# Performance work log

Measured on AMD Instinct MI355X. Metric: run time of the kernel, lower is better.

## Reference

```python
import jax, jax.numpy as jnp
import numpy as np

B, L, D1, D2 = 4, 2048, 1024, 1024

def setup_inputs() -> dict:
    key = jax.random.key(0)
    k1, k2, k3, k4, k5, k6 = jax.random.split(key, 6)
    s1 = 1.0 / np.sqrt(D1)
    s2 = 1.0 / np.sqrt(D2)
    return {
        "features_1": jax.random.normal(k1, (B, L, D1), dtype=jnp.float32),
        "features_2": jax.random.normal(k2, (B, L, D2), dtype=jnp.float32),
        # nn.Linear(d1, d2): W1 [d2, d1], b1 [d2]
        "W1": jax.random.uniform(k3, (D2, D1), jnp.float32, -s1, s1),
        "b1": jax.random.uniform(k4, (D2,), jnp.float32, -s1, s1),
        # nn.Linear(d2, d1): W2 [d1, d2], b2 [d1]
        "W2": jax.random.uniform(k5, (D1, D2), jnp.float32, -s2, s2),
        "b2": jax.random.uniform(k6, (D1,), jnp.float32, -s2, s2),
    }

def reference(features_1, features_2, W1, b1, W2, b2):
    # transformed_features_1: [B, L, D2]
    t1 = jnp.einsum('bld,ed->ble', features_1, W1) + b1
    # unscaled similarity: [B, L, L]
    sim = jnp.einsum('ble,bme->blm', t1, features_2)
    attn = jax.nn.softmax(sim, axis=-1)  # both softmaxes are identical
    attended_1 = jnp.einsum('blm,bme->ble', attn, features_2)  # [B, L, D2]
    attended_2 = jnp.einsum('blm,bme->ble', attn, t1)          # [B, L, D2]
    attended_2 = jnp.einsum('ble,de->bld', attended_2, W2) + b2  # [B, L, D1]
    return attended_1, attended_2
```

## Files before the change

### kernel.cpp

```cpp
#include <hip/hip_runtime.h>
#include <stdint.h>

#define BB 4
#define LL 2048
#define DD 1024

typedef __attribute__((ext_vector_type(4))) float f32x4;
typedef __attribute__((ext_vector_type(8))) _Float16 f16x8;
typedef __attribute__((ext_vector_type(4))) unsigned short u16x4;
typedef __attribute__((ext_vector_type(8))) unsigned short u16x8;
typedef unsigned short u16;

__device__ __forceinline__ u16 f2h(float x){
  return __builtin_bit_cast(u16, (_Float16)x);
}

__device__ __forceinline__ void gload16(const u16* g, u16* l){
  __builtin_amdgcn_global_load_lds((const __attribute__((address_space(1))) unsigned*)g,
                                   (__attribute__((address_space(3))) unsigned*)l,
                                   16, 0, 0);
}

__device__ __forceinline__ int xcd_swz(int bx, int nwg){
  return (bx & 7) * (nwg >> 3) + (bx >> 3);
}

__device__ __forceinline__ void stage_tile8(u16* lds, const u16* src, int ld, int wave, int lane){
  const int r0 = lane >> 3;
  const int cs = (((lane & 7) ^ r0) << 3);
  #pragma unroll
  for (int j = 0; j < 2; ++j){
    const int rb = wave*16 + j*8;
    gload16(src + (size_t)(rb + r0)*ld + cs, lds + rb*64);
  }
}

__device__ __forceinline__ void stage_fatA(u16* lds, const u16* src, int ld, int wave, int lane){
  const int r0 = lane >> 3;
  const int cs = (((lane & 7) ^ r0) << 3);
  #pragma unroll
  for (int j = 0; j < 8; ++j){
    const int rb = wave*64 + j*8;
    gload16(src + (size_t)(rb + r0)*ld + cs, lds + rb*64);
  }
}
__device__ __forceinline__ void stage_fatB(u16* lds, const u16* src, int ld, int wave, int lane){
  const int r0 = lane >> 3;
  const int cs = (((lane & 7) ^ r0) << 3);
  #pragma unroll
  for (int j = 0; j < 4; ++j){
    const int rb = wave*32 + j*8;
    gload16(src + (size_t)(rb + r0)*ld + cs, lds + rb*64);
  }
}

__device__ __forceinline__ f16x8 frag_ld(const u16* t, int row, int ko){
  return __builtin_bit_cast(f16x8,
    *reinterpret_cast<const f32x4*>(t + row*64 + (ko ^ ((row & 7) << 3))));
}

__global__ void cast3_k(const float* __restrict__ f1, u16* __restrict__ f1f,
                        const float* __restrict__ W1, u16* __restrict__ w1f,
                        const float* __restrict__ W2, u16* __restrict__ w2f){
  const int n1 = (BB*LL*DD)/4, nw = (DD*DD)/4;
  const int stride = gridDim.x * blockDim.x;
  for (int i = blockIdx.x*blockDim.x + threadIdx.x; i < n1 + 2*nw; i += stride){
    const float* s; u16* d; int k;
    if (i < n1){ s = f1; d = f1f; k = i; }
    else if (i < n1 + nw){ s = W1; d = w1f; k = i - n1; }
    else { s = W2; d = w2f; k = i - n1 - nw; }
    f32x4 v = reinterpret_cast<const f32x4*>(s)[k];
    u16x4 h;
    #pragma unroll
    for (int j = 0; j < 4; ++j) h[j] = f2h(v[j]);
    reinterpret_cast<u16x4*>(d)[k] = h;
  }
}

__global__ void castT_k(const float* __restrict__ f2, u16* __restrict__ f2f,
                        u16* __restrict__ f2T){
  __shared__ u16 t[32][33];
  const int b = blockIdx.z;
  const int d0 = blockIdx.x*32, l0 = blockIdx.y*32;
  const float* src = f2 + (size_t)b*LL*DD;
  u16* d1 = f2f + (size_t)b*LL*DD;
  u16* d2 = f2T + (size_t)b*DD*LL;
  const int x = threadIdx.x;
  for (int j = threadIdx.y; j < 32; j += 8){
    u16 h = f2h(src[(size_t)(l0+j)*DD + d0 + x]);
    d1[(size_t)(l0+j)*DD + d0 + x] = h;
    t[j][x] = h;
  }
  __syncthreads();
  for (int j = threadIdx.y; j < 32; j += 8)
    d2[(size_t)(d0+j)*LL + l0 + x] = t[x][j];
}

__global__ __launch_bounds__(512,4) void gemm_t1_k(
    const u16* __restrict__ A_g, const u16* __restrict__ B_g,
    const float* __restrict__ bias, u16* __restrict__ Oh){
  __shared__ __align__(16) u16 As[128*64];
  __shared__ __align__(16) u16 Bs[128*64];
  const int bx = xcd_swz(blockIdx.x, gridDim.x);
  const int bm = bx >> 3, bn = bx & 7;
  const int tid = threadIdx.x, wave = tid>>6, lane = tid&63;
  const int wr = wave>>2, wc = wave&3;
  const u16* Ab = A_g + (size_t)(bm*128)*DD;
  const u16* Bb = B_g + (size_t)(bn*128)*DD;
  f32x4 acc[4][2];
  #pragma unroll
  for (int i=0;i<4;i++)
    #pragma unroll
    for (int j=0;j<2;j++) acc[i][j] = (f32x4){0.f,0.f,0.f,0.f};

  for (int k0 = 0; k0 < DD; k0 += 64){
    __syncthreads();
    stage_tile8(As, Ab + k0, DD, wave, lane);
    stage_tile8(Bs, Bb + k0, DD, wave, lane);
    __syncthreads();
    #pragma unroll
    for (int kk=0;kk<2;kk++){
      const int ko = kk*32 + ((lane>>4)<<3);
      f16x8 a[4], bb[2];
      #pragma unroll
      for (int mi=0;mi<4;mi++) a[mi]  = frag_ld(As, wr*64 + mi*16 + (lane&15), ko);
      #pragma unroll
      for (int ni=0;ni<2;ni++) bb[ni] = frag_ld(Bs, wc*32 + ni*16 + (lane&15), ko);
      #pragma unroll
      for (int mi=0;mi<4;mi++)
        #pragma unroll
        for (int ni=0;ni<2;ni++)
          acc[mi][ni] = __builtin_amdgcn_mfma_f32_16x16x32_f16(a[mi], bb[ni], acc[mi][ni], 0,0,0);
    }
  }
  #pragma unroll
  for (int mi=0;mi<4;mi++)
    #pragma unroll
    for (int ni=0;ni<2;ni++){
      const int r = bm*128 + wr*64 + mi*16 + ((lane>>4)<<2);
      const int c = bn*128 + wc*32 + ni*16 + (lane&15);
      const float bv = bias[c];
      #pragma unroll
      for (int j=0;j<4;j++)
        Oh[(size_t)(r+j)*DD + c] = f2h(acc[mi][ni][j] + bv);
    }
}

__global__ __launch_bounds__(512,4) void gemm_zt_k(const u16* __restrict__ t1f,
                                                   const u16* __restrict__ w2f,
                                                   u16* __restrict__ ZT){
  __shared__ __align__(16) u16 As[128*64];
  __shared__ __align__(16) u16 Bs[128*64];
  __shared__ u16 T[128*132];
  const int bx = xcd_swz(blockIdx.x, gridDim.x);
  const int bm = bx >> 3, bn = bx & 7;
  const int tid = threadIdx.x, wave = tid>>6, lane = tid&63;
  const int wr = wave>>2, wc = wave&3;
  const u16* Ab = t1f + (size_t)(bm*128)*DD;
  const u16* Bb = w2f + (size_t)(bn*128)*DD;
  f32x4 acc[4][2];
  #pragma unroll
  for (int i=0;i<4;i++)
    #pragma unroll
    for (int j=0;j<2;j++) acc[i][j] = (f32x4){0.f,0.f,0.f,0.f};

  for (int k0 = 0; k0 < DD; k0 += 64){
    __syncthreads();
    stage_tile8(As, Ab + k0, DD, wave, lane);
    stage_tile8(Bs, Bb + k0, DD, wave, lane);
    __syncthreads();
    #pragma unroll
    for (int kk=0;kk<2;kk++){
      const int ko = kk*32 + ((lane>>4)<<3);
      f16x8 a[4], bb[2];
      #pragma unroll
      for (int mi=0;mi<4;mi++) a[mi]  = frag_ld(As, wr*64 + mi*16 + (lane&15), ko);
      #pragma unroll
      for (int ni=0;ni<2;ni++) bb[ni] = frag_ld(Bs, wc*32 + ni*16 + (lane&15), ko);
      #pragma unroll
      for (int mi=0;mi<4;mi++)
        #pragma unroll
        for (int ni=0;ni<2;ni++)
          acc[mi][ni] = __builtin_amdgcn_mfma_f32_16x16x32_f16(a[mi], bb[ni], acc[mi][ni], 0,0,0);
    }
  }
  #pragma unroll
  for (int mi=0;mi<4;mi++)
    #pragma unroll
    for (int ni=0;ni<2;ni++){
      const int r = wr*64 + mi*16 + ((lane>>4)<<2);
      const int c = wc*32 + ni*16 + (lane&15);
      #pragma unroll
      for (int j=0;j<4;j++)
        T[(r+j)*132 + c] = f2h(acc[mi][ni][j]);
    }
  __syncthreads();
  const int b2i = bm >> 4;
  const int mb  = (bm*128) & 2047;
  const int d   = tid >> 2, m0 = (tid & 3) << 5;
  u16* dst = ZT + ((size_t)b2i*DD + bn*128 + d)*LL + mb + m0;
  #pragma unroll
  for (int g = 0; g < 4; ++g){
    u16x8 v;
    #pragma unroll
    for (int e = 0; e < 8; ++e) v[e] = T[(m0 + g*8 + e)*132 + d];
    *reinterpret_cast<u16x8*>(dst + g*8) = v;
  }
}

__global__ __launch_bounds__(256) void softmax_k(float* __restrict__ sim){
  const int row = blockIdx.x;
  float* p = sim + (size_t)row * LL;
  const int tid = threadIdx.x, wave = tid>>6, lane = tid&63;
  f32x4 x0 = reinterpret_cast<const f32x4*>(p)[tid];
  f32x4 x1 = reinterpret_cast<const f32x4*>(p)[tid + 256];
  float mx = fmaxf(fmaxf(fmaxf(x0[0],x0[1]), fmaxf(x0[2],x0[3])),
                   fmaxf(fmaxf(x1[0],x1[1]), fmaxf(x1[2],x1[3])));
  #pragma unroll
  for (int o = 32; o; o >>= 1) mx = fmaxf(mx, __shfl_xor(mx, o, 64));
  __shared__ float red[8];
  if (lane == 0) red[wave] = mx;
  __syncthreads();
  mx = fmaxf(fmaxf(red[0], red[1]), fmaxf(red[2], red[3]));
  float e0[4], e1[4], s = 0.f;
  #pragma unroll
  for (int j=0;j<4;j++){ e0[j] = __expf(x0[j]-mx); s += e0[j]; }
  #pragma unroll
  for (int j=0;j<4;j++){ e1[j] = __expf(x1[j]-mx); s += e1[j]; }
  #pragma unroll
  for (int o = 32; o; o >>= 1) s += __shfl_xor(s, o, 64);
  if (lane == 0) red[4+wave] = s;
  __syncthreads();
  s = (red[4]+red[5]) + (red[6]+red[7]);
  const float inv = 1.0f / s;
  u16* ob = reinterpret_cast<u16*>(p);
  u16x4 w0, w1;
  #pragma unroll
  for (int j=0;j<4;j++){ w0[j] = f2h(e0[j]*inv); w1[j] = f2h(e1[j]*inv); }
  reinterpret_cast<u16x4*>(ob)[tid]       = w0;
  reinterpret_cast<u16x4*>(ob)[tid + 256] = w1;
}

template<int EPI>
__global__ __launch_bounds__(256,2) void gemmf_k(
    const u16* __restrict__ A_g, long long sAb, int lda,
    const u16* __restrict__ B0_g, const u16* __restrict__ B1_g, long long sBb, int ldb,
    float* __restrict__ C0, float* __restrict__ C1, long long sCb, int ldc,
    const float* __restrict__ bias, int K, int tn_sh){
  __shared__ __align__(16) u16 As[256*64];
  __shared__ __align__(16) u16 Bs[128*64];
  const int b = blockIdx.y;
  const int bx = xcd_swz(blockIdx.x, gridDim.x);
  const int bm = bx >> tn_sh, bn = bx & ((1 << tn_sh) - 1);
  const int tid = threadIdx.x, wave = tid>>6, lane = tid&63;
  const int wm = wave >> 1, wn = wave & 1;
  const u16* Ab = A_g + (size_t)b*sAb + (size_t)(bm*256)*lda;
  const u16* Bb;
  if (EPI == 0){
    Bb = B0_g + (size_t)b*sBb + (size_t)(bn*128)*ldb;
  } else {
    Bb = ((bn < 8) ? B0_g : B1_g) + (size_t)b*sBb + (size_t)((bn&7)*128)*ldb;
  }
  f32x4 acc[8][4];
  #pragma unroll
  for (int i=0;i<8;i++)
    #pragma unroll
    for (int j=0;j<4;j++) acc[i][j] = (f32x4){0.f,0.f,0.f,0.f};

  for (int k0 = 0; k0 < K; k0 += 64){
    __syncthreads();
    stage_fatA(As, Ab + k0, lda, wave, lane);
    stage_fatB(Bs, Bb + k0, ldb, wave, lane);
    __syncthreads();
    #pragma unroll
    for (int kk=0;kk<2;kk++){
      const int ko = kk*32 + ((lane>>4)<<3);
      f16x8 af[8], bf[4];
      #pragma unroll
      for (int mi=0;mi<8;mi++) af[mi] = frag_ld(As, wm*128 + mi*16 + (lane&15), ko);
      #pragma unroll
      for (int ni=0;ni<4;ni++) bf[ni] = frag_ld(Bs, wn*64 + ni*16 + (lane&15), ko);
      #pragma unroll
      for (int mi=0;mi<8;mi++)
        #pragma unroll
        for (int ni=0;ni<4;ni++)
          acc[mi][ni] = __builtin_amdgcn_mfma_f32_16x16x32_f16(af[mi], bf[ni], acc[mi][ni], 0,0,0);
    }
  }

  if (EPI == 0){
    float* Cb = C0 + (size_t)b*sCb;
    #pragma unroll
    for (int mi=0;mi<8;mi++)
      #pragma unroll
      for (int ni=0;ni<4;ni++){
        const int r = bm*256 + wm*128 + mi*16 + ((lane>>4)<<2);
        const int c = bn*128 + wn*64 + ni*16 + (lane&15);
        #pragma unroll
        for (int j=0;j<4;j++)
          Cb[(size_t)(r+j)*ldc + c] = acc[mi][ni][j];
      }
  } else {
    float* O = ((bn < 8) ? C0 : C1) + (size_t)b*sCb;
    const bool has_bias = (bn >= 8);
    #pragma unroll
    for (int mi=0;mi<8;mi++)
      #pragma unroll
      for (int ni=0;ni<4;ni++){
        const int r = bm*256 + wm*128 + mi*16 + ((lane>>4)<<2);
        const int c = (bn&7)*128 + wn*64 + ni*16 + (lane&15);
        const float bv = has_bias ? bias[c] : 0.f;
        #pragma unroll
        for (int j=0;j<4;j++)
          O[(size_t)(r+j)*ldc + c] = acc[mi][ni][j] + bv;
      }
  }
}

extern "C" void kernel_launch(void* const* d_in, const int* in_sizes, int n_in,
                              void* d_out, int out_size, void* d_ws, size_t ws_size,
                              hipStream_t stream) {
  const float* f1 = (const float*)d_in[0];
  const float* f2 = (const float*)d_in[1];
  const float* W1 = (const float*)d_in[2];
  const float* b1 = (const float*)d_in[3];
  const float* W2 = (const float*)d_in[4];
  const float* b2 = (const float*)d_in[5];
  float* out1 = (float*)d_out;
  float* out2 = out1 + (size_t)BB*LL*DD;

  char* ws = (char*)d_ws;
  u16* t1f = (u16*)(ws + 0);
  u16* ZT  = (u16*)(ws + 16777216);
  u16* f2f = (u16*)(ws + 33554432);
  u16* f2T = (u16*)(ws + 50331648);
  u16* w1f = (u16*)(ws + 67108864);
  u16* w2f = (u16*)(ws + 69206016);
  float* sim = (float*)(ws + 71303168);
  u16* f1f = (u16*)(ws + 71303168);

  castT_k<<<dim3(32, 64, BB), dim3(32, 8), 0, stream>>>(f2, f2f, f2T);
  cast3_k<<<4096, 256, 0, stream>>>(f1, f1f, W1, w1f, W2, w2f);
  gemm_t1_k<<<dim3(512, 1), 512, 0, stream>>>(f1f, w1f, b1, t1f);
  gemmf_k<0><<<dim3(128, BB), 256, 0, stream>>>(t1f, (long long)LL*DD, DD,
                                                f2f, nullptr, (long long)LL*DD, DD,
                                                sim, nullptr, (long long)LL*LL, LL,
                                                nullptr, DD, 4);
  softmax_k<<<BB*LL, 256, 0, stream>>>(sim);
  gemm_zt_k<<<dim3(512, 1), 512, 0, stream>>>(t1f, w2f, ZT);
  gemmf_k<1><<<dim3(128, BB), 256, 0, stream>>>((const u16*)sim, (long long)LL*4096, 4096,
                                                f2T, ZT, (long long)DD*LL, LL,
                                                out1, out2, (long long)LL*DD, DD,
                                                b2, LL, 4);
}
```

Measured before the change: 194.8 us.

## Prefetch next K-tile in gemmf_k by preloading A fragments and double-buffering B

Restructures the gemmf_k main loop so each wave first loads all A fragments for the current K tile into registers. It then issues the async global-to-LDS loads for the next A tile and the next B tile while running MFMAs on the current B buffer. B is double-buffered in shared memory, while A reuses a single buffer because its fragments are already held in registers. The aim is to overlap global memory latency with compute, at the cost of more VGPRs (16 A fragments held) and more LDS, which may lower occupancy under launch_bounds(256,2).

```diff
diff --git a/kernel.cpp b/kernel.cpp
--- a/kernel.cpp
+++ b/kernel.cpp
@@ -248,7 +248,7 @@
     float* __restrict__ C0, float* __restrict__ C1, long long sCb, int ldc,
     const float* __restrict__ bias, int K, int tn_sh){
   __shared__ __align__(16) u16 As[256*64];
-  __shared__ __align__(16) u16 Bs[128*64];
+  __shared__ __align__(16) u16 Bs[2][128*64];
   const int b = blockIdx.y;
   const int bx = xcd_swz(blockIdx.x, gridDim.x);
   const int bm = bx >> tn_sh, bn = bx & ((1 << tn_sh) - 1);
@@ -267,25 +267,37 @@
     #pragma unroll
     for (int j=0;j<4;j++) acc[i][j] = (f32x4){0.f,0.f,0.f,0.f};
 
-  for (int k0 = 0; k0 < K; k0 += 64){
-    __syncthreads();
-    stage_fatA(As, Ab + k0, lda, wave, lane);
-    stage_fatB(Bs, Bb + k0, ldb, wave, lane);
-    __syncthreads();
-    #pragma unroll
-    for (int kk=0;kk<2;kk++){
-      const int ko = kk*32 + ((lane>>4)<<3);
-      f16x8 af[8], bf[4];
-      #pragma unroll
-      for (int mi=0;mi<8;mi++) af[mi] = frag_ld(As, wm*128 + mi*16 + (lane&15), ko);
-      #pragma unroll
-      for (int ni=0;ni<4;ni++) bf[ni] = frag_ld(Bs, wn*64 + ni*16 + (lane&15), ko);
+  const int NT = K >> 6;
+  stage_fatA(As, Ab, lda, wave, lane);
+  stage_fatB(Bs[0], Bb, ldb, wave, lane);
+  __syncthreads();
+
+  for (int t = 0; t < NT; ++t){
+    f16x8 af[8][2];
+    #pragma unroll
+    for (int mi=0;mi<8;mi++)
+      #pragma unroll
+      for (int ks=0;ks<2;ks++)
+        af[mi][ks] = frag_ld(As, wm*128 + mi*16 + (lane&15), ks*32 + ((lane>>4)<<3));
+    __syncthreads();
+    if (t+1 < NT){
+      stage_fatA(As, Ab + (t+1)*64, lda, wave, lane);
+      stage_fatB(Bs[(t+1)&1], Bb + (t+1)*64, ldb, wave, lane);
+    }
+    const u16* Bcur = Bs[t&1];
+    #pragma unroll
+    for (int ks=0;ks<2;ks++){
+      const int ko = ks*32 + ((lane>>4)<<3);
+      f16x8 bf[4];
+      #pragma unroll
+      for (int ni=0;ni<4;ni++) bf[ni] = frag_ld(Bcur, wn*64 + ni*16 + (lane&15), ko);
       #pragma unroll
       for (int mi=0;mi<8;mi++)
         #pragma unroll
         for (int ni=0;ni<4;ni++)
-          acc[mi][ni] = __builtin_amdgcn_mfma_f32_16x16x32_f16(af[mi], bf[ni], acc[mi][ni], 0,0,0);
-    }
+          acc[mi][ni] = __builtin_amdgcn_mfma_f32_16x16x32_f16(af[mi][ks], bf[ni], acc[mi][ni], 0,0,0);
+    }
+    __syncthreads();
   }
 
   if (EPI == 0){
```

Result: slower. 198.7 us (+2.0%).

## Replace batched GEMMs with 8-wave 256x256 double-buffered pipelined kernel

Applied to the files above, without the earlier changes.

Replaces the 256x128-tile, 4-wave, single-buffered batched GEMM used for the similarity and attention-output products with a 256x256-tile, 8-wave kernel. The new kernel double-buffers the LDS tiles and splits each K step into four phases that interleave async global-to-LDS loads with MFMA bursts, using barriers, waitcnt and setprio. The aim is to hide global load latency and raise arithmetic intensity per block. The cost is 128KB of LDS per block and fewer blocks in the grid, which lowers occupancy and tail granularity.

```diff
diff --git a/kernel.cpp b/kernel.cpp
--- a/kernel.cpp
+++ b/kernel.cpp
@@ -31,25 +31,6 @@
   #pragma unroll
   for (int j = 0; j < 2; ++j){
     const int rb = wave*16 + j*8;
-    gload16(src + (size_t)(rb + r0)*ld + cs, lds + rb*64);
-  }
-}
-
-__device__ __forceinline__ void stage_fatA(u16* lds, const u16* src, int ld, int wave, int lane){
-  const int r0 = lane >> 3;
-  const int cs = (((lane & 7) ^ r0) << 3);
-  #pragma unroll
-  for (int j = 0; j < 8; ++j){
-    const int rb = wave*64 + j*8;
-    gload16(src + (size_t)(rb + r0)*ld + cs, lds + rb*64);
-  }
-}
-__device__ __forceinline__ void stage_fatB(u16* lds, const u16* src, int ld, int wave, int lane){
-  const int r0 = lane >> 3;
-  const int cs = (((lane & 7) ^ r0) << 3);
-  #pragma unroll
-  for (int j = 0; j < 4; ++j){
-    const int rb = wave*32 + j*8;
     gload16(src + (size_t)(rb + r0)*ld + cs, lds + rb*64);
   }
 }
@@ -242,50 +223,109 @@
 }
 
 template<int EPI>
-__global__ __launch_bounds__(256,2) void gemmf_k(
+__global__ __launch_bounds__(512,2) void gemm8_k(
     const u16* __restrict__ A_g, long long sAb, int lda,
     const u16* __restrict__ B0_g, const u16* __restrict__ B1_g, long long sBb, int ldb,
     float* __restrict__ C0, float* __restrict__ C1, long long sCb, int ldc,
-    const float* __restrict__ bias, int K, int tn_sh){
-  __shared__ __align__(16) u16 As[256*64];
-  __shared__ __align__(16) u16 Bs[128*64];
+    const float* __restrict__ bias, int K){
+  __shared__ __align__(16) u16 As[2][256*64];
+  __shared__ __align__(16) u16 Bs[2][256*64];
   const int b = blockIdx.y;
   const int bx = xcd_swz(blockIdx.x, gridDim.x);
-  const int bm = bx >> tn_sh, bn = bx & ((1 << tn_sh) - 1);
+  const int bm = bx >> 3, bn = bx & 7;
   const int tid = threadIdx.x, wave = tid>>6, lane = tid&63;
-  const int wm = wave >> 1, wn = wave & 1;
+  const int wm = wave >> 2, wn = wave & 3;
   const u16* Ab = A_g + (size_t)b*sAb + (size_t)(bm*256)*lda;
-  const u16* Bb;
-  if (EPI == 0){
-    Bb = B0_g + (size_t)b*sBb + (size_t)(bn*128)*ldb;
-  } else {
-    Bb = ((bn < 8) ? B0_g : B1_g) + (size_t)b*sBb + (size_t)((bn&7)*128)*ldb;
-  }
+  const u16* Bb = (EPI == 0)
+      ? (B0_g + (size_t)b*sBb + (size_t)(bn*256)*ldb)
+      : (((bn < 4) ? B0_g : B1_g) + (size_t)b*sBb + (size_t)((bn&3)*256)*ldb);
   f32x4 acc[8][4];
   #pragma unroll
   for (int i=0;i<8;i++)
     #pragma unroll
     for (int j=0;j<4;j++) acc[i][j] = (f32x4){0.f,0.f,0.f,0.f};
 
-  for (int k0 = 0; k0 < K; k0 += 64){
-    __syncthreads();
-    stage_fatA(As, Ab + k0, lda, wave, lane);
-    stage_fatB(Bs, Bb + k0, ldb, wave, lane);
-    __syncthreads();
-    #pragma unroll
-    for (int kk=0;kk<2;kk++){
-      const int ko = kk*32 + ((lane>>4)<<3);
-      f16x8 af[8], bf[4];
-      #pragma unroll
-      for (int mi=0;mi<8;mi++) af[mi] = frag_ld(As, wm*128 + mi*16 + (lane&15), ko);
-      #pragma unroll
-      for (int ni=0;ni<4;ni++) bf[ni] = frag_ld(Bs, wn*64 + ni*16 + (lane&15), ko);
-      #pragma unroll
-      for (int mi=0;mi<8;mi++)
-        #pragma unroll
-        for (int ni=0;ni<4;ni++)
-          acc[mi][ni] = __builtin_amdgcn_mfma_f32_16x16x32_f16(af[mi], bf[ni], acc[mi][ni], 0,0,0);
-    }
+  const int NT = K >> 6;
+  auto stA = [&](int tt, int h){
+    stage_tile8(&As[tt&1][h*8192], Ab + (size_t)(h*128)*lda + tt*64, lda, wave, lane);
+  };
+  auto stB = [&](int tt, int h){
+    stage_tile8(&Bs[tt&1][h*8192], Bb + (size_t)(h*128)*ldb + tt*64, ldb, wave, lane);
+  };
+
+  stA(0,0); stB(0,0); stA(0,1); stB(0,1);
+  stA(1,0); stB(1,0);
+  asm volatile("s_waitcnt vmcnt(4)" ::: "memory");
+  __builtin_amdgcn_s_barrier();
+
+  for (int t = 0; t < NT; ++t){
+    const u16* Ap = As[t&1];
+    const u16* Bp = Bs[t&1];
+    const int ar = wm*128 + (lane&15);
+    const int br = wn*64 + (lane&15);
+    const int k0 = ((lane>>4)<<3);
+    const int k1 = 32 + k0;
+    f16x8 af0[8], af1[8], bf0[4], bf1[4];
+
+    #pragma unroll
+    for (int mi=0;mi<8;mi++) af0[mi] = frag_ld(Ap, ar + mi*16, k0);
+    #pragma unroll
+    for (int ni=0;ni<4;ni++) bf0[ni] = frag_ld(Bp, br + ni*16, k0);
+    if (t+1 < NT) stA(t+1, 1);
+    __builtin_amdgcn_s_barrier();
+    asm volatile("s_waitcnt lgkmcnt(0)" ::: "memory");
+    __builtin_amdgcn_sched_barrier(0);
+    __builtin_amdgcn_s_setprio(1);
+    #pragma unroll
+    for (int mi=0;mi<4;mi++)
+      #pragma unroll
+      for (int ni=0;ni<4;ni++)
+        acc[mi][ni] = __builtin_amdgcn_mfma_f32_16x16x32_f16(af0[mi], bf0[ni], acc[mi][ni], 0,0,0);
+    __builtin_amdgcn_s_setprio(0);
+    __builtin_amdgcn_s_barrier();
+
+    #pragma unroll
+    for (int mi=0;mi<8;mi++) af1[mi] = frag_ld(Ap, ar + mi*16, k1);
+    if (t+1 < NT) stB(t+1, 1);
+    __builtin_amdgcn_s_barrier();
+    asm volatile("s_waitcnt lgkmcnt(0)" ::: "memory");
+    __builtin_amdgcn_sched_barrier(0);
+    __builtin_amdgcn_s_setprio(1);
+    #pragma unroll
+    for (int mi=4;mi<8;mi++)
+      #pragma unroll
+      for (int ni=0;ni<4;ni++)
+        acc[mi][ni] = __builtin_amdgcn_mfma_f32_16x16x32_f16(af0[mi], bf0[ni], acc[mi][ni], 0,0,0);
+    __builtin_amdgcn_s_setprio(0);
+    __builtin_amdgcn_s_barrier();
+
+    #pragma unroll
+    for (int ni=0;ni<4;ni++) bf1[ni] = frag_ld(Bp, br + ni*16, k1);
+    if (t+2 < NT) stA(t+2, 0);
+    __builtin_amdgcn_s_barrier();
+    asm volatile("s_waitcnt lgkmcnt(0)" ::: "memory");
+    __builtin_amdgcn_sched_barrier(0);
+    __builtin_amdgcn_s_setprio(1);
+    #pragma unroll
+    for (int mi=0;mi<4;mi++)
+      #pragma unroll
+      for (int ni=0;ni<4;ni++)
+        acc[mi][ni] = __builtin_amdgcn_mfma_f32_16x16x32_f16(af1[mi], bf1[ni], acc[mi][ni], 0,0,0);
+    __builtin_amdgcn_s_setprio(0);
+    __builtin_amdgcn_s_barrier();
+
+    if (t+2 < NT){ stB(t+2, 0); asm volatile("s_waitcnt vmcnt(4)" ::: "memory"); }
+    else         {              asm volatile("s_waitcnt vmcnt(0)" ::: "memory"); }
+    __builtin_amdgcn_s_barrier();
+    __builtin_amdgcn_sched_barrier(0);
+    __builtin_amdgcn_s_setprio(1);
+    #pragma unroll
+    for (int mi=4;mi<8;mi++)
+      #pragma unroll
+      for (int ni=0;ni<4;ni++)
+        acc[mi][ni] = __builtin_amdgcn_mfma_f32_16x16x32_f16(af1[mi], bf1[ni], acc[mi][ni], 0,0,0);
+    __builtin_amdgcn_s_setprio(0);
+    __builtin_amdgcn_s_barrier();
   }
 
   if (EPI == 0){
@@ -295,20 +335,20 @@
       #pragma unroll
       for (int ni=0;ni<4;ni++){
         const int r = bm*256 + wm*128 + mi*16 + ((lane>>4)<<2);
-        const int c = bn*128 + wn*64 + ni*16 + (lane&15);
+        const int c = bn*256 + wn*64 + ni*16 + (lane&15);
         #pragma unroll
         for (int j=0;j<4;j++)
           Cb[(size_t)(r+j)*ldc + c] = acc[mi][ni][j];
       }
   } else {
-    float* O = ((bn < 8) ? C0 : C1) + (size_t)b*sCb;
-    const bool has_bias = (bn >= 8);
+    float* O = ((bn < 4) ? C0 : C1) + (size_t)b*sCb;
+    const bool has_bias = (bn >= 4);
     #pragma unroll
     for (int mi=0;mi<8;mi++)
       #pragma unroll
       for (int ni=0;ni<4;ni++){
         const int r = bm*256 + wm*128 + mi*16 + ((lane>>4)<<2);
-        const int c = (bn&7)*128 + wn*64 + ni*16 + (lane&15);
+        const int c = (bn&3)*256 + wn*64 + ni*16 + (lane&15);
         const float bv = has_bias ? bias[c] : 0.f;
         #pragma unroll
         for (int j=0;j<4;j++)
@@ -342,14 +382,14 @@
   castT_k<<<dim3(32, 64, BB), dim3(32, 8), 0, stream>>>(f2, f2f, f2T);
   cast3_k<<<4096, 256, 0, stream>>>(f1, f1f, W1, w1f, W2, w2f);
   gemm_t1_k<<<dim3(512, 1), 512, 0, stream>>>(f1f, w1f, b1, t1f);
-  gemmf_k<0><<<dim3(128, BB), 256, 0, stream>>>(t1f, (long long)LL*DD, DD,
-                                                f2f, nullptr, (long long)LL*DD, DD,
-                                                sim, nullptr, (long long)LL*LL, LL,
-                                                nullptr, DD, 4);
+  gemm8_k<0><<<dim3(64, BB), 512, 0, stream>>>(t1f, (long long)LL*DD, DD,
+                                               f2f, nullptr, (long long)LL*DD, DD,
+                                               sim, nullptr, (long long)LL*LL, LL,
+                                               nullptr, DD);
   softmax_k<<<BB*LL, 256, 0, stream>>>(sim);
   gemm_zt_k<<<dim3(512, 1), 512, 0, stream>>>(t1f, w2f, ZT);
-  gemmf_k<1><<<dim3(128, BB), 256, 0, stream>>>((const u16*)sim, (long long)LL*4096, 4096,
-                                                f2T, ZT, (long long)DD*LL, LL,
-                                                out1, out2, (long long)LL*DD, DD,
-                                                b2, LL, 4);
-}
+  gemm8_k<1><<<dim3(64, BB), 512, 0, stream>>>((const u16*)sim, (long long)LL*4096, 4096,
+                                               f2T, ZT, (long long)DD*LL, LL,
+                                               out1, out2, (long long)LL*DD, DD,
+                                               b2, LL);
+}
```

After: 201.8 us. +3.6%, slower.

## Store similarity matrix in fp16 and merge the cast kernels into one launch

Applied to the files above, without the earlier changes.

The similarity GEMM now writes fp16 logits instead of fp32, and softmax reads and writes fp16 in place. This halves the traffic of the largest intermediate and makes the PV GEMM's A operand dense with stride L. The f2 transpose-cast and the f1/W1/W2 casts are also merged into one launch via an extra grid z slice, removing a kernel launch. Rounding unscaled logits to fp16 before softmax loses precision, and large logits could overflow the fp16 range.

```diff
diff --git a/kernel.cpp b/kernel.cpp
--- a/kernel.cpp
+++ b/kernel.cpp
@@ -14,6 +14,9 @@
 __device__ __forceinline__ u16 f2h(float x){
   return __builtin_bit_cast(u16, (_Float16)x);
 }
+__device__ __forceinline__ float h2f(u16 h){
+  return (float)__builtin_bit_cast(_Float16, h);
+}
 
 __device__ __forceinline__ void gload16(const u16* g, u16* l){
   __builtin_amdgcn_global_load_lds((const __attribute__((address_space(1))) unsigned*)g,
@@ -59,41 +62,44 @@
     *reinterpret_cast<const f32x4*>(t + row*64 + (ko ^ ((row & 7) << 3))));
 }
 
-__global__ void cast3_k(const float* __restrict__ f1, u16* __restrict__ f1f,
-                        const float* __restrict__ W1, u16* __restrict__ w1f,
-                        const float* __restrict__ W2, u16* __restrict__ w2f){
-  const int n1 = (BB*LL*DD)/4, nw = (DD*DD)/4;
-  const int stride = gridDim.x * blockDim.x;
-  for (int i = blockIdx.x*blockDim.x + threadIdx.x; i < n1 + 2*nw; i += stride){
-    const float* s; u16* d; int k;
-    if (i < n1){ s = f1; d = f1f; k = i; }
-    else if (i < n1 + nw){ s = W1; d = w1f; k = i - n1; }
-    else { s = W2; d = w2f; k = i - n1 - nw; }
-    f32x4 v = reinterpret_cast<const f32x4*>(s)[k];
-    u16x4 h;
-    #pragma unroll
-    for (int j = 0; j < 4; ++j) h[j] = f2h(v[j]);
-    reinterpret_cast<u16x4*>(d)[k] = h;
-  }
-}
-
-__global__ void castT_k(const float* __restrict__ f2, u16* __restrict__ f2f,
-                        u16* __restrict__ f2T){
+__global__ void cast_all_k(const float* __restrict__ f2, u16* __restrict__ f2f,
+                           u16* __restrict__ f2T,
+                           const float* __restrict__ f1, u16* __restrict__ f1f,
+                           const float* __restrict__ W1, u16* __restrict__ w1f,
+                           const float* __restrict__ W2, u16* __restrict__ w2f){
   __shared__ u16 t[32][33];
-  const int b = blockIdx.z;
-  const int d0 = blockIdx.x*32, l0 = blockIdx.y*32;
-  const float* src = f2 + (size_t)b*LL*DD;
-  u16* d1 = f2f + (size_t)b*LL*DD;
-  u16* d2 = f2T + (size_t)b*DD*LL;
-  const int x = threadIdx.x;
-  for (int j = threadIdx.y; j < 32; j += 8){
-    u16 h = f2h(src[(size_t)(l0+j)*DD + d0 + x]);
-    d1[(size_t)(l0+j)*DD + d0 + x] = h;
-    t[j][x] = h;
-  }
-  __syncthreads();
-  for (int j = threadIdx.y; j < 32; j += 8)
-    d2[(size_t)(d0+j)*LL + l0 + x] = t[x][j];
+  const int z = blockIdx.z;
+  if (z < 4){
+    const int d0 = blockIdx.x*32, l0 = blockIdx.y*32;
+    const float* src = f2 + (size_t)z*LL*DD;
+    u16* d1 = f2f + (size_t)z*LL*DD;
+    u16* d2 = f2T + (size_t)z*DD*LL;
+    const int x = threadIdx.x;
+    for (int j = threadIdx.y; j < 32; j += 8){
+      u16 h = f2h(src[(size_t)(l0+j)*DD + d0 + x]);
+      d1[(size_t)(l0+j)*DD + d0 + x] = h;
+      t[j][x] = h;
+    }
+    __syncthreads();
+    for (int j = threadIdx.y; j < 32; j += 8)
+      d2[(size_t)(d0+j)*LL + l0 + x] = t[x][j];
+  } else {
+    const int n1 = (BB*LL*DD)/4, nw = (DD*DD)/4;
+    const int ntot = n1 + 2*nw;
+    const int base = (blockIdx.y*32 + blockIdx.x)*256 + threadIdx.y*32 + threadIdx.x;
+    const int stride = 2048*256;
+    for (int i = base; i < ntot; i += stride){
+      const float* s; u16* d; int k;
+      if (i < n1){ s = f1; d = f1f; k = i; }
+      else if (i < n1 + nw){ s = W1; d = w1f; k = i - n1; }
+      else { s = W2; d = w2f; k = i - n1 - nw; }
+      f32x4 v = reinterpret_cast<const f32x4*>(s)[k];
+      u16x4 h;
+      #pragma unroll
+      for (int j = 0; j < 4; ++j) h[j] = f2h(v[j]);
+      reinterpret_cast<u16x4*>(d)[k] = h;
+    }
+  }
 }
 
 __global__ __launch_bounds__(512,4) void gemm_t1_k(
@@ -208,37 +214,35 @@
   }
 }
 
-__global__ __launch_bounds__(256) void softmax_k(float* __restrict__ sim){
+__global__ __launch_bounds__(256) void softmax_k(u16* __restrict__ sim){
   const int row = blockIdx.x;
-  float* p = sim + (size_t)row * LL;
+  u16* p = sim + (size_t)row * LL;
   const int tid = threadIdx.x, wave = tid>>6, lane = tid&63;
-  f32x4 x0 = reinterpret_cast<const f32x4*>(p)[tid];
-  f32x4 x1 = reinterpret_cast<const f32x4*>(p)[tid + 256];
-  float mx = fmaxf(fmaxf(fmaxf(x0[0],x0[1]), fmaxf(x0[2],x0[3])),
-                   fmaxf(fmaxf(x1[0],x1[1]), fmaxf(x1[2],x1[3])));
+  u16x8 v = reinterpret_cast<const u16x8*>(p)[tid];
+  float x[8];
+  #pragma unroll
+  for (int j=0;j<8;j++) x[j] = h2f(v[j]);
+  float mx = fmaxf(fmaxf(fmaxf(x[0],x[1]), fmaxf(x[2],x[3])),
+                   fmaxf(fmaxf(x[4],x[5]), fmaxf(x[6],x[7])));
   #pragma unroll
   for (int o = 32; o; o >>= 1) mx = fmaxf(mx, __shfl_xor(mx, o, 64));
   __shared__ float red[8];
   if (lane == 0) red[wave] = mx;
   __syncthreads();
   mx = fmaxf(fmaxf(red[0], red[1]), fmaxf(red[2], red[3]));
-  float e0[4], e1[4], s = 0.f;
-  #pragma unroll
-  for (int j=0;j<4;j++){ e0[j] = __expf(x0[j]-mx); s += e0[j]; }
-  #pragma unroll
-  for (int j=0;j<4;j++){ e1[j] = __expf(x1[j]-mx); s += e1[j]; }
+  float e[8], s = 0.f;
+  #pragma unroll
+  for (int j=0;j<8;j++){ e[j] = __expf(x[j]-mx); s += e[j]; }
   #pragma unroll
   for (int o = 32; o; o >>= 1) s += __shfl_xor(s, o, 64);
   if (lane == 0) red[4+wave] = s;
   __syncthreads();
   s = (red[4]+red[5]) + (red[6]+red[7]);
   const float inv = 1.0f / s;
-  u16* ob = reinterpret_cast<u16*>(p);
-  u16x4 w0, w1;
-  #pragma unroll
-  for (int j=0;j<4;j++){ w0[j] = f2h(e0[j]*inv); w1[j] = f2h(e1[j]*inv); }
-  reinterpret_cast<u16x4*>(ob)[tid]       = w0;
-  reinterpret_cast<u16x4*>(ob)[tid + 256] = w1;
+  u16x8 w;
+  #pragma unroll
+  for (int j=0;j<8;j++) w[j] = f2h(e[j]*inv);
+  reinterpret_cast<u16x8*>(p)[tid] = w;
 }
 
 template<int EPI>
@@ -256,10 +260,10 @@
   const int wm = wave >> 1, wn = wave & 1;
   const u16* Ab = A_g + (size_t)b*sAb + (size_t)(bm*256)*lda;
   const u16* Bb;
-  if (EPI == 0){
+  if (EPI == 1){
+    Bb = ((bn < 8) ? B0_g : B1_g) + (size_t)b*sBb + (size_t)((bn&7)*128)*ldb;
+  } else {
     Bb = B0_g + (size_t)b*sBb + (size_t)(bn*128)*ldb;
-  } else {
-    Bb = ((bn < 8) ? B0_g : B1_g) + (size_t)b*sBb + (size_t)((bn&7)*128)*ldb;
   }
   f32x4 acc[8][4];
   #pragma unroll
@@ -299,6 +303,18 @@
         #pragma unroll
         for (int j=0;j<4;j++)
           Cb[(size_t)(r+j)*ldc + c] = acc[mi][ni][j];
+      }
+  } else if (EPI == 2){
+    u16* Oh = reinterpret_cast<u16*>(C0) + (size_t)b*sCb;
+    #pragma unroll
+    for (int mi=0;mi<8;mi++)
+      #pragma unroll
+      for (int ni=0;ni<4;ni++){
+        const int r = bm*256 + wm*128 + mi*16 + ((lane>>4)<<2);
+        const int c = bn*128 + wn*64 + ni*16 + (lane&15);
+        #pragma unroll
+        for (int j=0;j<4;j++)
+          Oh[(size_t)(r+j)*ldc + c] = f2h(acc[mi][ni][j]);
       }
   } else {
     float* O = ((bn < 8) ? C0 : C1) + (size_t)b*sCb;
@@ -336,19 +352,19 @@
   u16* f2T = (u16*)(ws + 50331648);
   u16* w1f = (u16*)(ws + 67108864);
   u16* w2f = (u16*)(ws + 69206016);
-  float* sim = (float*)(ws + 71303168);
+  u16* sim = (u16*)(ws + 71303168);
   u16* f1f = (u16*)(ws + 71303168);
 
-  castT_k<<<dim3(32, 64, BB), dim3(32, 8), 0, stream>>>(f2, f2f, f2T);
-  cast3_k<<<4096, 256, 0, stream>>>(f1, f1f, W1, w1f, W2, w2f);
+  cast_all_k<<<dim3(32, 64, 5), dim3(32, 8), 0, stream>>>(f2, f2f, f2T,
+                                                          f1, f1f, W1, w1f, W2, w2f);
   gemm_t1_k<<<dim3(512, 1), 512, 0, stream>>>(f1f, w1f, b1, t1f);
-  gemmf_k<0><<<dim3(128, BB), 256, 0, stream>>>(t1f, (long long)LL*DD, DD,
+  gemmf_k<2><<<dim3(128, BB), 256, 0, stream>>>(t1f, (long long)LL*DD, DD,
                                                 f2f, nullptr, (long long)LL*DD, DD,
-                                                sim, nullptr, (long long)LL*LL, LL,
+                                                (float*)sim, nullptr, (long long)LL*LL, LL,
                                                 nullptr, DD, 4);
   softmax_k<<<BB*LL, 256, 0, stream>>>(sim);
   gemm_zt_k<<<dim3(512, 1), 512, 0, stream>>>(t1f, w2f, ZT);
-  gemmf_k<1><<<dim3(128, BB), 256, 0, stream>>>((const u16*)sim, (long long)LL*4096, 4096,
+  gemmf_k<1><<<dim3(128, BB), 256, 0, stream>>>(sim, (long long)LL*LL, LL,
                                                 f2T, ZT, (long long)DD*LL, LL,
                                                 out1, out2, (long long)LL*DD, DD,
                                                 b2, LL, 4);
```

Result: faster. 186.6 us (-4.2%).
